# Kernel tuning notes

Hardware: AMD Instinct MI355X
Metric: run time of the kernel (lower is better)

Reference implementation:

```python
import jax, jax.numpy as jnp
import numpy as np

N_NODES = 100000
N_EDGES = 1600000
IN_C, HID_C, OUT_C = 128, 128, 64


def setup_inputs() -> dict:
    key = jax.random.key(0)
    ks = jax.random.split(key, 6)
    x = jax.random.normal(ks[0], (N_NODES, IN_C), dtype=jnp.float32)
    edge_index = jax.random.randint(ks[1], (2, N_EDGES), 0, N_NODES)
    W1 = jax.random.normal(ks[2], (IN_C, HID_C), dtype=jnp.float32) * (1.0 / np.sqrt(IN_C))
    b1 = jnp.zeros((HID_C,), dtype=jnp.float32)
    W2 = jax.random.normal(ks[3], (HID_C, OUT_C), dtype=jnp.float32) * (1.0 / np.sqrt(HID_C))
    b2 = jnp.zeros((OUT_C,), dtype=jnp.float32)
    return {"x": x, "edge_index": edge_index, "W1": W1, "b1": b1, "W2": W2, "b2": b2}


def gcn_conv(x, W, b, src, dst):
    # PyG GCNConv: D^{-1/2} (A + I) D^{-1/2} X W + b, with self-loops handled
    # analytically (no explicit self-loop edges materialized).
    h = x @ W                                             # [N, d_out]
    ones = jnp.ones(src.shape[0], dtype=h.dtype)
    deg = jax.ops.segment_sum(ones, dst, num_segments=N_NODES) + 1.0  # +1 self-loop
    dinv = jax.lax.rsqrt(deg)                             # deg >= 1, safe
    norm = dinv[src] * dinv[dst]                          # [E]
    msg = h[src] * norm[:, None]                          # gather + scale  [E, d_out]
    agg = jax.ops.segment_sum(msg, dst, num_segments=N_NODES)
    agg = agg + h * (dinv * dinv)[:, None]                # self-loop contribution
    return agg + b


def reference(x, edge_index, W1, b1, W2, b2):
    src, dst = edge_index[0], edge_index[1]
    h = jax.nn.relu(gcn_conv(x, W1, b1, src, dst))
    # dropout is identity in eval mode
    out = gcn_conv(h, W2, b2, src, dst)
    return out
```

## Files before the change

kernel.cpp:

```cpp
#include <hip/hip_runtime.h>

#define N_NODESC 100000
#define N_EDGESC 1600000
#define NB_BUCKETS 391
#define BUCKET_CAP 5120
#define CHUNK_A 8192

typedef __attribute__((ext_vector_type(4))) float floatx4;
typedef __attribute__((ext_vector_type(8))) short shortx8;

__device__ __forceinline__ unsigned short f32_to_bf16_rne(float f) {
    unsigned int u = __float_as_uint(f);
    unsigned int r = u + 0x7fffu + ((u >> 16) & 1u);
    return (unsigned short)(r >> 16);
}
__device__ __forceinline__ float bf16_to_f32(unsigned short h) {
    return __uint_as_float(((unsigned int)h) << 16);
}
__device__ __forceinline__ float bflo(unsigned int u) { return __uint_as_float(u << 16); }
__device__ __forceinline__ float bfhi(unsigned int u) { return __uint_as_float(u & 0xffff0000u); }
__device__ __forceinline__ unsigned int pack2bf(float a, float b) {
    return ((unsigned int)f32_to_bf16_rne(b) << 16) | (unsigned int)f32_to_bf16_rne(a);
}

__global__ __launch_bounds__(256) void k_wfrag_all(const float* __restrict__ W1,
        const float* __restrict__ W2,
        unsigned short* __restrict__ w1hi, unsigned short* __restrict__ w1lo,
        unsigned short* __restrict__ w2hi, unsigned short* __restrict__ w2lo,
        int* __restrict__ gcur) {
    int t = threadIdx.x;
    if (blockIdx.x == 0)
        for (int i = t; i < NB_BUCKETS; i += 256) gcur[i] = i * BUCKET_CAP;
    int idx = blockIdx.x * 256 + t;
    float f;
    int k, col, C, o;
    unsigned short *phi, *plo;
    if (idx < 16384) {
        k = idx >> 7; col = idx & 127; C = 8;
        f = W1[idx]; phi = w1hi; plo = w1lo;
    } else {
        int idx2 = idx - 16384;
        k = idx2 >> 6; col = idx2 & 63; C = 4;
        f = W2[idx2]; phi = w2hi; plo = w2lo;
    }
    unsigned short hi = f32_to_bf16_rne(f);
    unsigned short lo = f32_to_bf16_rne(f - bf16_to_f32(hi));
    int kc = k >> 5, q = (k >> 3) & 3, j = k & 7;
    int c = col >> 4, n = col & 15;
    o = (((kc * C + c) * 4 + q) * 16 + n) * 8 + j;
    phi[o] = hi; plo[o] = lo;
}

__global__ __launch_bounds__(256) void k_bucket(const int* __restrict__ src,
        const int* __restrict__ dst, int* __restrict__ gcur,
        unsigned int* __restrict__ tmp) {
    __shared__ int hist[NB_BUCKETS];
    int t = threadIdx.x;
    for (int i = t; i < NB_BUCKETS; i += 256) hist[i] = 0;
    __syncthreads();
    int base = blockIdx.x * CHUNK_A;
    int end = min(base + CHUNK_A, N_EDGESC);
    for (int e = base + t; e < end; e += 256)
        atomicAdd(&hist[dst[e] >> 8], 1);
    __syncthreads();
    for (int i = t; i < NB_BUCKETS; i += 256) {
        int c = hist[i];
        hist[i] = (c > 0) ? atomicAdd(&gcur[i], c) : 0;
    }
    __syncthreads();
    for (int e = base + t; e < end; e += 256) {
        int d = dst[e];
        int pos = atomicAdd(&hist[d >> 8], 1);
        tmp[pos] = ((unsigned int)src[e] << 8) | (unsigned int)(d & 255);
    }
}

__global__ __launch_bounds__(256) void k_place(const unsigned int* __restrict__ tmp,
        const int* __restrict__ gcur,
        int* __restrict__ swsrc, int* __restrict__ deg,
        int* __restrict__ row_ptr, float* __restrict__ dinv) {
    __shared__ int hist[256], scan[256], lcur[256];
    int b = blockIdx.x, t = threadIdx.x;
    int start = b * BUCKET_CAP;
    int end = gcur[b];
    hist[t] = 0;
    __syncthreads();
    for (int i = start + t; i < end; i += 256)
        atomicAdd(&hist[tmp[i] & 255u], 1);
    __syncthreads();
    int own = hist[t];
    scan[t] = own;
    __syncthreads();
    for (int off = 1; off < 256; off <<= 1) {
        int add = (t >= off) ? scan[t - off] : 0;
        __syncthreads();
        scan[t] += add;
        __syncthreads();
    }
    int rp = start + scan[t] - own;
    lcur[t] = rp;
    int node = (b << 8) + t;
    if (node < N_NODESC) {
        deg[node] = own;
        row_ptr[node] = rp;
        dinv[node] = rsqrtf((float)own + 1.0f);
    }
    __syncthreads();
    for (int i = start + t; i < end; i += 256) {
        unsigned int v = tmp[i];
        int pos = atomicAdd(&lcur[v & 255u], 1);
        swsrc[pos] = (int)(v >> 8);
    }
}

template<int NOUT, int AFP32>
__global__ __launch_bounds__(256) void k_gemm_mfma(const void* __restrict__ Xv,
        const unsigned short* __restrict__ whi, const unsigned short* __restrict__ wlo,
        const float* __restrict__ dinv, unsigned short* __restrict__ H) {
    constexpr int C = NOUT / 16;
    constexpr int PITCH = NOUT + 4;
    __shared__ __align__(16) float etile[4][16][PITCH];
    int wv = threadIdx.x >> 6, lane = threadIdx.x & 63;
    int n16 = lane & 15, q = lane >> 4;
    int rowBase = blockIdx.x * 128 + wv * 32;
    floatx4 acc[2][C];
#pragma unroll
    for (int m = 0; m < 2; ++m)
#pragma unroll
        for (int c = 0; c < C; ++c) acc[m][c] = (floatx4){0.f, 0.f, 0.f, 0.f};

    const shortx8* whi8 = (const shortx8*)whi;
    const shortx8* wlo8 = (const shortx8*)wlo;

    for (int kc = 0; kc < 4; ++kc) {
        shortx8 ahi[2], alo[2];
#pragma unroll
        for (int m = 0; m < 2; ++m) {
            int r = rowBase + m * 16 + n16;
            if (r >= N_NODESC) r = N_NODESC - 1;
            if (AFP32) {
                const float* xp = &((const float*)Xv)[(size_t)r * 128 + kc * 32 + q * 8];
                floatx4 x0 = *(const floatx4*)xp;
                floatx4 x1 = *(const floatx4*)(xp + 4);
#pragma unroll
                for (int jj = 0; jj < 4; ++jj) {
                    unsigned short h0 = f32_to_bf16_rne(x0[jj]);
                    ahi[m][jj] = (short)h0;
                    alo[m][jj] = (short)f32_to_bf16_rne(x0[jj] - bf16_to_f32(h0));
                    unsigned short h1 = f32_to_bf16_rne(x1[jj]);
                    ahi[m][jj + 4] = (short)h1;
                    alo[m][jj + 4] = (short)f32_to_bf16_rne(x1[jj] - bf16_to_f32(h1));
                }
            } else {
                const unsigned short* xp = &((const unsigned short*)Xv)[(size_t)r * 128 + kc * 32 + q * 8];
                ahi[m] = *(const shortx8*)xp;
            }
        }
#pragma unroll
        for (int c = 0; c < C; ++c) {
            int fo = (kc * C + c) * 64 + lane;
            shortx8 bhi = whi8[fo];
            shortx8 blo = wlo8[fo];
#pragma unroll
            for (int m = 0; m < 2; ++m) {
                acc[m][c] = __builtin_amdgcn_mfma_f32_16x16x32_bf16(ahi[m], bhi, acc[m][c], 0, 0, 0);
                if (AFP32)
                    acc[m][c] = __builtin_amdgcn_mfma_f32_16x16x32_bf16(alo[m], bhi, acc[m][c], 0, 0, 0);
                acc[m][c] = __builtin_amdgcn_mfma_f32_16x16x32_bf16(ahi[m], blo, acc[m][c], 0, 0, 0);
            }
        }
    }
    constexpr int CPL = NOUT / 4;
#pragma unroll
    for (int m = 0; m < 2; ++m) {
        __syncthreads();
#pragma unroll
        for (int c = 0; c < C; ++c)
#pragma unroll
            for (int reg = 0; reg < 4; ++reg)
                etile[wv][q * 4 + reg][c * 16 + n16] = acc[m][c][reg];
        __syncthreads();
        int row = lane >> 2, cb = lane & 3;
        int r = rowBase + m * 16 + row;
        if (r < N_NODESC) {
            float dv = dinv[r];
            unsigned int po[CPL / 2];
#pragma unroll
            for (int i = 0; i < CPL / 4; ++i) {
                floatx4 v = *(const floatx4*)&etile[wv][row][cb * CPL + i * 4];
                po[i * 2 + 0] = pack2bf(v[0] * dv, v[1] * dv);
                po[i * 2 + 1] = pack2bf(v[2] * dv, v[3] * dv);
            }
            unsigned int* op = (unsigned int*)&H[(size_t)r * NOUT + cb * CPL];
#pragma unroll
            for (int i = 0; i < CPL / 8; ++i)
                *(uint4*)(op + i * 4) = *(uint4*)&po[i * 4];
        }
    }
}

__global__ __launch_bounds__(256) void k_agg128(const unsigned short* __restrict__ Hb,
        const int* __restrict__ swsrc, const int* __restrict__ row_ptr,
        const int* __restrict__ deg, const float* __restrict__ dinv,
        const float* __restrict__ bias, unsigned short* __restrict__ outb) {
    int node = blockIdx.x * 4 + (threadIdx.x >> 6);
    int lane = threadIdx.x & 63;
    int g = lane >> 4, l16 = lane & 15;
    int start = row_ptr[node];
    int end = start + deg[node];
    float acc[8] = {0.f, 0.f, 0.f, 0.f, 0.f, 0.f, 0.f, 0.f};
    int j = start + g;
    for (; j + 4 < end; j += 8) {
        int s0 = swsrc[j];
        int s1 = swsrc[j + 4];
        uint4 v0 = *(const uint4*)(Hb + (size_t)s0 * 128 + l16 * 8);
        uint4 v1 = *(const uint4*)(Hb + (size_t)s1 * 128 + l16 * 8);
        acc[0] += bflo(v0.x) + bflo(v1.x);
        acc[1] += bfhi(v0.x) + bfhi(v1.x);
        acc[2] += bflo(v0.y) + bflo(v1.y);
        acc[3] += bfhi(v0.y) + bfhi(v1.y);
        acc[4] += bflo(v0.z) + bflo(v1.z);
        acc[5] += bfhi(v0.z) + bfhi(v1.z);
        acc[6] += bflo(v0.w) + bflo(v1.w);
        acc[7] += bfhi(v0.w) + bfhi(v1.w);
    }
    if (j < end) {
        int s0 = swsrc[j];
        uint4 v0 = *(const uint4*)(Hb + (size_t)s0 * 128 + l16 * 8);
        acc[0] += bflo(v0.x); acc[1] += bfhi(v0.x);
        acc[2] += bflo(v0.y); acc[3] += bfhi(v0.y);
        acc[4] += bflo(v0.z); acc[5] += bfhi(v0.z);
        acc[6] += bflo(v0.w); acc[7] += bfhi(v0.w);
    }
#pragma unroll
    for (int i = 0; i < 8; ++i) {
        acc[i] += __shfl_xor(acc[i], 16);
        acc[i] += __shfl_xor(acc[i], 32);
    }
    if (g == 0) {
        float dv = dinv[node];
        uint4 sv = *(const uint4*)(Hb + (size_t)node * 128 + l16 * 8);
        floatx4 b0 = *(const floatx4*)&bias[l16 * 8];
        floatx4 b1 = *(const floatx4*)&bias[l16 * 8 + 4];
        float o0 = dv * (acc[0] + bflo(sv.x)) + b0[0];
        float o1 = dv * (acc[1] + bfhi(sv.x)) + b0[1];
        float o2 = dv * (acc[2] + bflo(sv.y)) + b0[2];
        float o3 = dv * (acc[3] + bfhi(sv.y)) + b0[3];
        float o4 = dv * (acc[4] + bflo(sv.z)) + b1[0];
        float o5 = dv * (acc[5] + bfhi(sv.z)) + b1[1];
        float o6 = dv * (acc[6] + bflo(sv.w)) + b1[2];
        float o7 = dv * (acc[7] + bfhi(sv.w)) + b1[3];
        uint4 o;
        o.x = pack2bf(fmaxf(o0, 0.f), fmaxf(o1, 0.f));
        o.y = pack2bf(fmaxf(o2, 0.f), fmaxf(o3, 0.f));
        o.z = pack2bf(fmaxf(o4, 0.f), fmaxf(o5, 0.f));
        o.w = pack2bf(fmaxf(o6, 0.f), fmaxf(o7, 0.f));
        *(uint4*)(outb + (size_t)node * 128 + l16 * 8) = o;
    }
}

__global__ __launch_bounds__(256) void k_agg64(const unsigned short* __restrict__ Hb,
        const int* __restrict__ swsrc, const int* __restrict__ row_ptr,
        const int* __restrict__ deg, const float* __restrict__ dinv,
        const float* __restrict__ bias, float* __restrict__ out) {
    int node = blockIdx.x * 4 + (threadIdx.x >> 6);
    int lane = threadIdx.x & 63;
    int g = lane >> 3, l8 = lane & 7;
    int start = row_ptr[node];
    int end = start + deg[node];
    float acc[8] = {0.f, 0.f, 0.f, 0.f, 0.f, 0.f, 0.f, 0.f};
    int j = start + g;
    for (; j + 8 < end; j += 16) {
        int s0 = swsrc[j];
        int s1 = swsrc[j + 8];
        uint4 v0 = *(const uint4*)(Hb + (size_t)s0 * 64 + l8 * 8);
        uint4 v1 = *(const uint4*)(Hb + (size_t)s1 * 64 + l8 * 8);
        acc[0] += bflo(v0.x) + bflo(v1.x);
        acc[1] += bfhi(v0.x) + bfhi(v1.x);
        acc[2] += bflo(v0.y) + bflo(v1.y);
        acc[3] += bfhi(v0.y) + bfhi(v1.y);
        acc[4] += bflo(v0.z) + bflo(v1.z);
        acc[5] += bfhi(v0.z) + bfhi(v1.z);
        acc[6] += bflo(v0.w) + bflo(v1.w);
        acc[7] += bfhi(v0.w) + bfhi(v1.w);
    }
    if (j < end) {
        int s0 = swsrc[j];
        uint4 v0 = *(const uint4*)(Hb + (size_t)s0 * 64 + l8 * 8);
        acc[0] += bflo(v0.x); acc[1] += bfhi(v0.x);
        acc[2] += bflo(v0.y); acc[3] += bfhi(v0.y);
        acc[4] += bflo(v0.z); acc[5] += bfhi(v0.z);
        acc[6] += bflo(v0.w); acc[7] += bfhi(v0.w);
    }
#pragma unroll
    for (int i = 0; i < 8; ++i) {
        acc[i] += __shfl_xor(acc[i], 8);
        acc[i] += __shfl_xor(acc[i], 16);
        acc[i] += __shfl_xor(acc[i], 32);
    }
    if (g == 0) {
        float dv = dinv[node];
        uint4 sv = *(const uint4*)(Hb + (size_t)node * 64 + l8 * 8);
        floatx4 b0 = *(const floatx4*)&bias[l8 * 8];
        floatx4 b1 = *(const floatx4*)&bias[l8 * 8 + 4];
        floatx4 o0, o1;
        o0[0] = dv * (acc[0] + bflo(sv.x)) + b0[0];
        o0[1] = dv * (acc[1] + bfhi(sv.x)) + b0[1];
        o0[2] = dv * (acc[2] + bflo(sv.y)) + b0[2];
        o0[3] = dv * (acc[3] + bfhi(sv.y)) + b0[3];
        o1[0] = dv * (acc[4] + bflo(sv.z)) + b1[0];
        o1[1] = dv * (acc[5] + bfhi(sv.z)) + b1[1];
        o1[2] = dv * (acc[6] + bflo(sv.w)) + b1[2];
        o1[3] = dv * (acc[7] + bfhi(sv.w)) + b1[3];
        *(floatx4*)&out[(size_t)node * 64 + l8 * 8] = o0;
        *(floatx4*)&out[(size_t)node * 64 + l8 * 8 + 4] = o1;
    }
}

extern "C" void kernel_launch(void* const* d_in, const int* in_sizes, int n_in,
                              void* d_out, int out_size, void* d_ws, size_t ws_size,
                              hipStream_t stream) {
    const float* x  = (const float*)d_in[0];
    const int*   ei = (const int*)d_in[1];
    const float* W1 = (const float*)d_in[2];
    const float* b1 = (const float*)d_in[3];
    const float* W2 = (const float*)d_in[4];
    const float* b2 = (const float*)d_in[5];
    float* out = (float*)d_out;
    const int* src = ei;
    const int* dst = ei + N_EDGESC;

    char* ws = (char*)d_ws;
    size_t off = 0;
    auto alloc = [&](size_t bytes) -> void* {
        off = (off + 255) & ~(size_t)255;
        void* p = ws + off;
        off += bytes;
        return p;
    };
    const size_t CSR_SLOTS = (size_t)NB_BUCKETS * BUCKET_CAP;
    int*   deg     = (int*)  alloc((size_t)N_NODESC * 4);
    float* dinv    = (float*)alloc((size_t)N_NODESC * 4);
    int*   row_ptr = (int*)  alloc((size_t)N_NODESC * 4);
    int*   gcur    = (int*)  alloc(NB_BUCKETS * 4);
    unsigned int* tmp   = (unsigned int*)alloc(CSR_SLOTS * 4);
    int*   swsrc   = (int*)  alloc(CSR_SLOTS * 4);
    unsigned short* w1hi = (unsigned short*)alloc(128 * 128 * 2);
    unsigned short* w1lo = (unsigned short*)alloc(128 * 128 * 2);
    unsigned short* w2hi = (unsigned short*)alloc(128 * 64 * 2);
    unsigned short* w2lo = (unsigned short*)alloc(128 * 64 * 2);
    unsigned short* h1b  = (unsigned short*)alloc((size_t)N_NODESC * 128 * 2);
    unsigned short* hb   = (unsigned short*)alloc((size_t)N_NODESC * 128 * 2);
    unsigned short* h2b  = h1b;

    const int nbGemm = (N_NODESC + 127) / 128;
    const int nbBkt  = (N_EDGESC + CHUNK_A - 1) / CHUNK_A;

    k_wfrag_all<<<(16384 + 8192) / 256, 256, 0, stream>>>(W1, W2, w1hi, w1lo, w2hi, w2lo, gcur);
    k_bucket<<<nbBkt, 256, 0, stream>>>(src, dst, gcur, tmp);
    k_place<<<NB_BUCKETS, 256, 0, stream>>>(tmp, gcur, swsrc, deg, row_ptr, dinv);

    k_gemm_mfma<128, 1><<<nbGemm, 256, 0, stream>>>(x, w1hi, w1lo, dinv, h1b);
    k_agg128<<<N_NODESC / 4, 256, 0, stream>>>(h1b, swsrc, row_ptr, deg, dinv, b1, hb);
    k_gemm_mfma<64, 0><<<nbGemm, 256, 0, stream>>>(hb, w2hi, w2lo, dinv, h2b);
    k_agg64<<<N_NODESC / 4, 256, 0, stream>>>(h2b, swsrc, row_ptr, deg, dinv, b2, out);
}
```

Baseline: 296.4 us.

## Replace two-pass bucketed CSR build with global-atomic degree count and scatter

Replaces the bucket-then-place CSR construction (LDS histograms, a temp buffer and a second local sort pass) with three simple kernels: global atomic degree counting per node, a per-bucket scan producing row pointers and cursors, and a global atomic scatter of source indices. This removes the intermediate tmp buffer and its extra read/write pass. In exchange it relies on contended global atomics on 100k counters and random scattered writes, and edge order within a row becomes nondeterministic. It still assumes each 256-node bucket fits in BUCKET_CAP slots.

```diff
diff --git a/kernel.cpp b/kernel.cpp
--- a/kernel.cpp
+++ b/kernel.cpp
@@ -4,7 +4,6 @@
 #define N_EDGESC 1600000
 #define NB_BUCKETS 391
 #define BUCKET_CAP 5120
-#define CHUNK_A 8192
 
 typedef __attribute__((ext_vector_type(4))) float floatx4;
 typedef __attribute__((ext_vector_type(8))) short shortx8;
@@ -27,11 +26,10 @@
         const float* __restrict__ W2,
         unsigned short* __restrict__ w1hi, unsigned short* __restrict__ w1lo,
         unsigned short* __restrict__ w2hi, unsigned short* __restrict__ w2lo,
-        int* __restrict__ gcur) {
+        int* __restrict__ deg) {
     int t = threadIdx.x;
-    if (blockIdx.x == 0)
-        for (int i = t; i < NB_BUCKETS; i += 256) gcur[i] = i * BUCKET_CAP;
     int idx = blockIdx.x * 256 + t;
+    for (int i = idx; i < N_NODESC; i += 96 * 256) deg[i] = 0;
     float f;
     int k, col, C, o;
     unsigned short *phi, *plo;
@@ -51,44 +49,21 @@
     phi[o] = hi; plo[o] = lo;
 }
 
-__global__ __launch_bounds__(256) void k_bucket(const int* __restrict__ src,
-        const int* __restrict__ dst, int* __restrict__ gcur,
-        unsigned int* __restrict__ tmp) {
-    __shared__ int hist[NB_BUCKETS];
-    int t = threadIdx.x;
-    for (int i = t; i < NB_BUCKETS; i += 256) hist[i] = 0;
-    __syncthreads();
-    int base = blockIdx.x * CHUNK_A;
-    int end = min(base + CHUNK_A, N_EDGESC);
-    for (int e = base + t; e < end; e += 256)
-        atomicAdd(&hist[dst[e] >> 8], 1);
-    __syncthreads();
-    for (int i = t; i < NB_BUCKETS; i += 256) {
-        int c = hist[i];
-        hist[i] = (c > 0) ? atomicAdd(&gcur[i], c) : 0;
-    }
-    __syncthreads();
-    for (int e = base + t; e < end; e += 256) {
-        int d = dst[e];
-        int pos = atomicAdd(&hist[d >> 8], 1);
-        tmp[pos] = ((unsigned int)src[e] << 8) | (unsigned int)(d & 255);
-    }
-}
-
-__global__ __launch_bounds__(256) void k_place(const unsigned int* __restrict__ tmp,
-        const int* __restrict__ gcur,
-        int* __restrict__ swsrc, int* __restrict__ deg,
-        int* __restrict__ row_ptr, float* __restrict__ dinv) {
-    __shared__ int hist[256], scan[256], lcur[256];
+__global__ __launch_bounds__(256) void k_deg(const int* __restrict__ dst,
+        int* __restrict__ deg) {
+    int idx = blockIdx.x * 256 + threadIdx.x;
+    int stride = gridDim.x * 256;
+    for (int e = idx; e < N_EDGESC; e += stride)
+        atomicAdd(&deg[dst[e]], 1);
+}
+
+__global__ __launch_bounds__(256) void k_rowptr(const int* __restrict__ deg,
+        int* __restrict__ row_ptr, int* __restrict__ cursor,
+        float* __restrict__ dinv) {
+    __shared__ int scan[256];
     int b = blockIdx.x, t = threadIdx.x;
-    int start = b * BUCKET_CAP;
-    int end = gcur[b];
-    hist[t] = 0;
-    __syncthreads();
-    for (int i = start + t; i < end; i += 256)
-        atomicAdd(&hist[tmp[i] & 255u], 1);
-    __syncthreads();
-    int own = hist[t];
+    int node = (b << 8) + t;
+    int own = (node < N_NODESC) ? deg[node] : 0;
     scan[t] = own;
     __syncthreads();
     for (int off = 1; off < 256; off <<= 1) {
@@ -97,19 +72,23 @@
         scan[t] += add;
         __syncthreads();
     }
-    int rp = start + scan[t] - own;
-    lcur[t] = rp;
-    int node = (b << 8) + t;
     if (node < N_NODESC) {
-        deg[node] = own;
+        int rp = b * BUCKET_CAP + scan[t] - own;
         row_ptr[node] = rp;
+        cursor[node] = rp;
         dinv[node] = rsqrtf((float)own + 1.0f);
     }
-    __syncthreads();
-    for (int i = start + t; i < end; i += 256) {
-        unsigned int v = tmp[i];
-        int pos = atomicAdd(&lcur[v & 255u], 1);
-        swsrc[pos] = (int)(v >> 8);
+}
+
+__global__ __launch_bounds__(256) void k_scatter(const int* __restrict__ src,
+        const int* __restrict__ dst, int* __restrict__ cursor,
+        int* __restrict__ swsrc) {
+    int idx = blockIdx.x * 256 + threadIdx.x;
+    int stride = gridDim.x * 256;
+    for (int e = idx; e < N_EDGESC; e += stride) {
+        int d = dst[e];
+        int pos = atomicAdd(&cursor[d], 1);
+        swsrc[pos] = src[e];
     }
 }
 
@@ -342,8 +321,7 @@
     int*   deg     = (int*)  alloc((size_t)N_NODESC * 4);
     float* dinv    = (float*)alloc((size_t)N_NODESC * 4);
     int*   row_ptr = (int*)  alloc((size_t)N_NODESC * 4);
-    int*   gcur    = (int*)  alloc(NB_BUCKETS * 4);
-    unsigned int* tmp   = (unsigned int*)alloc(CSR_SLOTS * 4);
+    int*   cursor  = (int*)  alloc((size_t)N_NODESC * 4);
     int*   swsrc   = (int*)  alloc(CSR_SLOTS * 4);
     unsigned short* w1hi = (unsigned short*)alloc(128 * 128 * 2);
     unsigned short* w1lo = (unsigned short*)alloc(128 * 128 * 2);
@@ -354,11 +332,12 @@
     unsigned short* h2b  = h1b;
 
     const int nbGemm = (N_NODESC + 127) / 128;
-    const int nbBkt  = (N_EDGESC + CHUNK_A - 1) / CHUNK_A;
-
-    k_wfrag_all<<<(16384 + 8192) / 256, 256, 0, stream>>>(W1, W2, w1hi, w1lo, w2hi, w2lo, gcur);
-    k_bucket<<<nbBkt, 256, 0, stream>>>(src, dst, gcur, tmp);
-    k_place<<<NB_BUCKETS, 256, 0, stream>>>(tmp, gcur, swsrc, deg, row_ptr, dinv);
+    const int nbEdge = 2048;
+
+    k_wfrag_all<<<(16384 + 8192) / 256, 256, 0, stream>>>(W1, W2, w1hi, w1lo, w2hi, w2lo, deg);
+    k_deg<<<nbEdge, 256, 0, stream>>>(dst, deg);
+    k_rowptr<<<NB_BUCKETS, 256, 0, stream>>>(deg, row_ptr, cursor, dinv);
+    k_scatter<<<nbEdge, 256, 0, stream>>>(src, dst, cursor, swsrc);
 
     k_gemm_mfma<128, 1><<<nbGemm, 256, 0, stream>>>(x, w1hi, w1lo, dinv, h1b);
     k_agg128<<<N_NODESC / 4, 256, 0, stream>>>(h1b, swsrc, row_ptr, deg, dinv, b1, hb);
```

Measured after the change: 443.9 us. +49.7%, slower.
